# Optimization experiments

Hardware: AMD Instinct MI355X
Metric: run time of the kernel (lower is better)

Reference implementation:

```python
import jax, jax.numpy as jnp
import numpy as np

H = 16          # query heads
KV = 8          # kv heads
D = 256         # head_dim
HID = 3584      # hidden_size
ROPE_BASE = 10000.0
SCALING = 256.0 ** -0.5          # query_pre_attn_scalar ** -0.5
SOFTCAP = 50.0                   # attn_logit_softcapping
WINDOW = 1536 - 1                # sliding_window - 1 (layer_idx 0 is even)


def _rope_neox(x, positions):
    # x: [T, nh, D]; neox style: rotate the two halves of the head dim
    half = D // 2
    inv_freq = 1.0 / (ROPE_BASE ** (jnp.arange(0, D, 2, dtype=jnp.float32) / D))  # [half]
    freqs = positions.astype(jnp.float32)[:, None] * inv_freq[None, :]            # [T, half]
    cos = jnp.cos(freqs)[:, None, :]  # [T, 1, half]
    sin = jnp.sin(freqs)[:, None, :]
    x1, x2 = x[..., :half], x[..., half:]
    return jnp.concatenate([x1 * cos - x2 * sin, x2 * cos + x1 * sin], axis=-1)


def setup_inputs() -> dict:
    key = jax.random.key(0)
    k1, k2, k3 = jax.random.split(key, 3)
    T = 3072
    hidden_states = jax.random.normal(k1, (T, HID), dtype=jnp.float32)
    w_qkv = jax.random.normal(k2, (H * D + 2 * KV * D, HID), dtype=jnp.float32) * 0.02
    w_o = jax.random.normal(k3, (HID, H * D), dtype=jnp.float32) * 0.02
    positions = jnp.arange(T, dtype=jnp.int64)
    return {"positions": positions, "hidden_states": hidden_states,
            "w_qkv": w_qkv, "w_o": w_o}


def reference(positions, hidden_states, w_qkv, w_o):
    T = hidden_states.shape[0]
    qkv = hidden_states @ w_qkv.T                       # [T, (H+2KV)*D]
    q, k, v = jnp.split(qkv, [H * D, H * D + KV * D], axis=-1)
    q = q.reshape(T, H, D)
    k = k.reshape(T, KV, D)
    v = v.reshape(T, KV, D)
    q = _rope_neox(q, positions)
    k = _rope_neox(k, positions)
    # GQA: repeat kv heads (2 query heads per kv head)
    k = jnp.repeat(k, H // KV, axis=1)                  # [T, H, D]
    v = jnp.repeat(v, H // KV, axis=1)
    scores = jnp.einsum('thd,shd->hts', q, k) * SCALING  # [H, T, T]
    scores = SOFTCAP * jnp.tanh(scores / SOFTCAP)       # logit softcapping
    i = positions[:, None]
    j = positions[None, :]
    mask = (j <= i) & (i - j <= WINDOW)                 # causal + sliding window
    scores = jnp.where(mask[None, :, :], scores, -jnp.inf)
    probs = jax.nn.softmax(scores, axis=-1)
    attn = jnp.einsum('hts,shd->thd', probs, v).reshape(T, H * D)
    return attn @ w_o.T                                 # [T, HID]
```

## Files before the change

### kernel.cpp

```cpp
#include <hip/hip_runtime.h>
#include <math.h>

typedef unsigned short u16;
typedef __attribute__((ext_vector_type(8))) short short8;
typedef __attribute__((ext_vector_type(4))) float f32x4;
typedef __attribute__((ext_vector_type(4))) unsigned short u16x4;

#define HN 16
#define KVH 8
#define DH 256
#define HID 3584
#define T_LEN 3072
#define QKV_N 8192
#define O_N 4096
#define WIN 1535
#define SCALING 0.0625f
#define SOFTCAP 50.0f
#define KOFF 4096
#define VOFF 6144
#define PSTR 72
#define NJT 48
#define M_FIX 20.0f

__device__ __forceinline__ u16 f2bf(float f) {
  unsigned u = __float_as_uint(f);
  u += 0x7FFFu + ((u >> 16) & 1u);
  return (u16)(u >> 16);
}
__device__ __forceinline__ float bf2f(u16 b) {
  return __uint_as_float(((unsigned)b) << 16);
}

__device__ __forceinline__ void gload_lds16(const void* g, void* l) {
  __builtin_amdgcn_global_load_lds(
      (const __attribute__((address_space(1))) void*)g,
      (__attribute__((address_space(3))) void*)l, 16, 0, 0);
}

__device__ __forceinline__ f32x4 mfma_bf16(short8 a, short8 b, f32x4 c) {
  return __builtin_amdgcn_mfma_f32_16x16x32_bf16(a, b, c, 0, 0, 0);
}

#define BARX()                                  \
  do {                                          \
    __builtin_amdgcn_sched_barrier(0);          \
    __builtin_amdgcn_s_barrier();               \
    __builtin_amdgcn_sched_barrier(0);          \
  } while (0)

__global__ __launch_bounds__(256) void cvt2_kernel(const float* __restrict__ a,
                                                   u16* __restrict__ da, int nva,
                                                   const float* __restrict__ b,
                                                   u16* __restrict__ db, int nvb) {
  int v = blockIdx.x * 256 + threadIdx.x;
  const float* src;
  u16* dst;
  if (v < nva) {
    src = a + (size_t)v * 4;
    dst = da + (size_t)v * 4;
  } else if (v < nva + nvb) {
    int u = v - nva;
    src = b + (size_t)u * 4;
    dst = db + (size_t)u * 4;
  } else {
    return;
  }
  float4 x = *(const float4*)src;
  u16x4 o;
  o[0] = f2bf(x.x); o[1] = f2bf(x.y); o[2] = f2bf(x.z); o[3] = f2bf(x.w);
  *(u16x4*)dst = o;
}

template <int OUT_BF16>
__global__ __launch_bounds__(512, 2) void gemm8p(const u16* __restrict__ A,
                                                 const u16* __restrict__ B,
                                                 void* __restrict__ Cv,
                                                 int N, int K, int ntn, int cpx,
                                                 int gemmBlocks,
                                                 float* __restrict__ rtab) {
  __shared__ u16 sA[2][256 * 64];
  __shared__ u16 sB[2][256 * 64];

  const int bid = blockIdx.x;
  const int tid = threadIdx.x;

  if (bid >= gemmBlocks) {
    const int rb = bid - gemmBlocks;
    for (int idx = rb * 512 + tid; idx < T_LEN * 128; idx += 128 * 512) {
      int d = idx & 127;
      int t = idx >> 7;
      float inv = exp2f((float)d * (-13.287712379549449f / 128.0f));
      float ang = (float)t * inv;
      float2 cs;
      cs.x = cosf(ang);
      cs.y = sinf(ang);
      *(float2*)(rtab + (size_t)idx * 2) = cs;
    }
    return;
  }

  const int wg = (bid & 7) * cpx + (bid >> 3);
  const int bm = wg / ntn, bn = wg % ntn;
  const int row0 = bm * 256, col0 = bn * 256;
  const int lane = tid & 63, wid = tid >> 6;
  const int wr = wid >> 2, wc = wid & 3;
  const int NT = K >> 6;

  const int srow = lane >> 3;
  const int sg = (lane & 7) ^ srow;

  auto stage = [&](int tau, int kind) {
    if (tau >= NT) return;
    const int b = tau & 1;
    const int rbase = (kind & 1) * 128;
    const u16* src;
    u16* dst;
    if (kind >= 2) {
      src = A + (size_t)(row0 + rbase + wid * 8 + srow) * K + (size_t)tau * 64 + sg * 8;
      dst = &sA[b][(rbase + wid * 8) * 64];
    } else {
      src = B + (size_t)(col0 + rbase + wid * 8 + srow) * K + (size_t)tau * 64 + sg * 8;
      dst = &sB[b][(rbase + wid * 8) * 64];
    }
    gload_lds16(src, dst);
    gload_lds16(src + (size_t)64 * K, dst + 64 * 64);
  };

  f32x4 acc[8][4] = {};
  const int fr = lane & 15;
  const int fh = fr & 7;
  const int gk0 = (lane >> 4) ^ fh;
  const int gk1 = ((lane >> 4) + 4) ^ fh;

  stage(0, 0); stage(0, 1); stage(0, 2); stage(0, 3);
  stage(1, 0); stage(1, 1); stage(1, 2);
  __builtin_amdgcn_sched_barrier(0);
  asm volatile("s_waitcnt vmcnt(6)" ::: "memory");
  BARX();

  for (int u = 0; u < NT; ++u) {
    const int b = u & 1;
    const u16* pA = &sA[b][0];
    const u16* pB = &sB[b][0];
    short8 bf[4][2], afA[2][2], afB[2][2];

#define LDB_(ni, kk) (*(const short8*)&pB[(wc * 64 + (ni)*16 + fr) * 64 + (kk ? gk1 : gk0) * 8])
#define LDA_(mi, kk) (*(const short8*)&pA[(wr * 128 + (mi)*16 + fr) * 64 + (kk ? gk1 : gk0) * 8])
#define MFMA2(AF, mi0)                                                   \
  __builtin_amdgcn_s_setprio(1);                                        \
  _Pragma("unroll") for (int ni = 0; ni < 4; ++ni) {                    \
    acc[mi0][ni] = mfma_bf16(AF[0][0], bf[ni][0], acc[mi0][ni]);        \
    acc[mi0][ni] = mfma_bf16(AF[0][1], bf[ni][1], acc[mi0][ni]);        \
    acc[mi0 + 1][ni] = mfma_bf16(AF[1][0], bf[ni][0], acc[mi0 + 1][ni]);\
    acc[mi0 + 1][ni] = mfma_bf16(AF[1][1], bf[ni][1], acc[mi0 + 1][ni]);\
  }                                                                      \
  __builtin_amdgcn_s_setprio(0);                                        \
  asm volatile("s_waitcnt lgkmcnt(0)" ::: "memory");

#pragma unroll
    for (int ni = 0; ni < 4; ++ni) { bf[ni][0] = LDB_(ni, 0); bf[ni][1] = LDB_(ni, 1); }
    afA[0][0] = LDA_(0, 0); afA[0][1] = LDA_(0, 1);
    afA[1][0] = LDA_(1, 0); afA[1][1] = LDA_(1, 1);
    stage(u + 1, 3);
    BARX();
    MFMA2(afA, 0);
    BARX();
    afA[0][0] = LDA_(2, 0); afA[0][1] = LDA_(2, 1);
    afA[1][0] = LDA_(3, 0); afA[1][1] = LDA_(3, 1);
    stage(u + 2, 0);
    BARX();
    MFMA2(afA, 2);
    BARX();
    afA[0][0] = LDA_(4, 0); afA[0][1] = LDA_(4, 1);
    afA[1][0] = LDA_(5, 0); afA[1][1] = LDA_(5, 1);
    afB[0][0] = LDA_(6, 0); afB[0][1] = LDA_(6, 1);
    afB[1][0] = LDA_(7, 0); afB[1][1] = LDA_(7, 1);
    stage(u + 2, 1);
    BARX();
    MFMA2(afA, 4);
    BARX();
    stage(u + 2, 2);
    __builtin_amdgcn_sched_barrier(0);
    if (u + 2 < NT) {
      asm volatile("s_waitcnt vmcnt(6)" ::: "memory");
    } else {
      asm volatile("s_waitcnt vmcnt(0)" ::: "memory");
    }
    BARX();
    MFMA2(afB, 6);
    BARX();
#undef LDB_
#undef LDA_
#undef MFMA2
  }

#pragma unroll
  for (int mi = 0; mi < 8; ++mi) {
#pragma unroll
    for (int ni = 0; ni < 4; ++ni) {
      const int r = row0 + wr * 128 + mi * 16 + (lane >> 4) * 4;
      const int c = col0 + wc * 64 + ni * 16 + (lane & 15);
#pragma unroll
      for (int j = 0; j < 4; ++j) {
        float v = acc[mi][ni][j];
        if (OUT_BF16)
          ((u16*)Cv)[(size_t)(r + j) * N + c] = f2bf(v);
        else
          ((float*)Cv)[(size_t)(r + j) * N + c] = v;
      }
    }
  }
}

__global__ __launch_bounds__(256) void rope_kernel(u16* __restrict__ qkv,
                                                   const float* __restrict__ tab) {
  int idx = blockIdx.x * 256 + threadIdx.x;
  int d = idx & 127;
  int hh = (idx >> 7) % 24;
  int t = idx / (24 * 128);
  if (t >= T_LEN) return;
  size_t base = (size_t)t * QKV_N + (hh < HN ? hh * DH : HN * DH + (hh - HN) * DH);
  float2 cs = *(const float2*)(tab + ((size_t)(t << 7) + d) * 2);
  float x1 = bf2f(qkv[base + d]);
  float x2 = bf2f(qkv[base + d + 128]);
  qkv[base + d] = f2bf(x1 * cs.x - x2 * cs.y);
  qkv[base + d + 128] = f2bf(x2 * cs.x + x1 * cs.y);
}

__global__ __launch_bounds__(256) void vtrans_kernel(const u16* __restrict__ qkv,
                                                     u16* __restrict__ vt) {
  __shared__ u16 tile[256 * 72];
  const int jb = blockIdx.x * 64;
  const int kvh = blockIdx.y;
  const int tid = threadIdx.x;
  const int t = tid & 63, dc = tid >> 6;

  const u16* src = qkv + (size_t)(jb + t) * QKV_N + VOFF + kvh * DH + dc * 64;
#pragma unroll
  for (int i = 0; i < 8; ++i) {
    short8 v = *(const short8*)(src + i * 8);
    int d0 = dc * 64 + i * 8;
#pragma unroll
    for (int j = 0; j < 8; ++j) tile[(d0 + j) * 72 + t] = (u16)(short)v[j];
  }
  __syncthreads();

  u16* dst = vt + ((size_t)kvh * NJT + blockIdx.x) * 16384;
#pragma unroll
  for (int s = 0; s < 8; ++s) {
    int G = s * 256 + tid;
    int d = G >> 3, g = G & 7;
    short8 x = *(const short8*)&tile[d * 72 + ((g ^ (d & 7)) * 8)];
    *(short8*)(dst + G * 8) = x;
  }
}

__global__ __launch_bounds__(256) void attn_kernel(const u16* __restrict__ qkv,
                                                   const u16* __restrict__ vt,
                                                   u16* __restrict__ po,
                                                   float* __restrict__ ml) {
  const int wg = blockIdx.x;
  const int kvh = wg & 7;
  const int rest = wg >> 3;
  const int qt = rest >> 2;
  const int c = (rest >> 1) & 1;
  const int h = kvh * 2 + (rest & 1);
  const int qb = qt * 64;
  const int tid = threadIdx.x, lane = tid & 63, w = tid >> 6;

  __shared__ u16 sK[64 * 256];
  __shared__ u16 sVt[64 * 256];
  __shared__ u16 sP[4][16 * PSTR];

  int jmin = qb - WIN; if (jmin < 0) jmin = 0;
  const int jt0 = jmin >> 6, jt1 = qb >> 6;
  const int nt = jt1 - jt0 + 1;
  const int half = (nt + 1) >> 1;
  const int t_beg = (c == 0) ? jt0 : jt0 + half;
  const int t_end = (c == 0) ? jt0 + half : jt1 + 1;

  const int qrow = qb + w * 16 + (lane & 15);
  short8 qf[8];
  {
    const u16* qp = qkv + (size_t)qrow * QKV_N + h * DH + (lane >> 4) * 8;
#pragma unroll
    for (int kc = 0; kc < 8; ++kc) qf[kc] = *(const short8*)(qp + kc * 32);
  }

  f32x4 O[16];
#pragma unroll
  for (int i = 0; i < 16; ++i) O[i] = f32x4{0.f, 0.f, 0.f, 0.f};
  float lrow[4] = {0.f, 0.f, 0.f, 0.f};

  const int dl = lane & 15;
  const int vb0 = dl * 64 + (((lane >> 4)) ^ (dl & 7)) * 8;
  const int vb1 = dl * 64 + (((lane >> 4) + 4) ^ (dl & 7)) * 8;

  for (int jt = t_beg; jt < t_end; ++jt) {
    const int jb = jt * 64;
#pragma unroll
    for (int i = 0; i < 8; ++i) {
      int rl = w * 16 + i * 2 + (lane >> 5);
      int g = (lane & 31) ^ (rl & 7);
      gload_lds16(qkv + (size_t)(jb + rl) * QKV_N + KOFF + kvh * DH + g * 8,
                  &sK[(w * 16 + i * 2) * 256]);
    }
    {
      const u16* vtile = vt + ((size_t)kvh * NJT + jt) * 16384;
#pragma unroll
      for (int s = 0; s < 8; ++s) {
        int id = w * 8 + s;
        gload_lds16(vtile + id * 512 + lane * 8, &sVt[id * 512]);
      }
    }
    __syncthreads();

    f32x4 S[4];
#pragma unroll
    for (int nf = 0; nf < 4; ++nf) S[nf] = f32x4{0.f, 0.f, 0.f, 0.f};
#pragma unroll
    for (int nf = 0; nf < 4; ++nf) {
      int krow = nf * 16 + (lane & 15);
#pragma unroll
      for (int kc = 0; kc < 8; ++kc) {
        int g = (kc * 4 + (lane >> 4)) ^ (krow & 7);
        short8 kf = *(const short8*)&sK[krow * 256 + g * 8];
        S[nf] = mfma_bf16(qf[kc], kf, S[nf]);
      }
    }

#pragma unroll
    for (int r = 0; r < 4; ++r) {
      const int irow = qb + w * 16 + (lane >> 4) * 4 + r;
      const int ql = (lane >> 4) * 4 + r;
#pragma unroll
      for (int nf = 0; nf < 4; ++nf) {
        int j = jb + nf * 16 + (lane & 15);
        float x = S[nf][r] * (SCALING / SOFTCAP);
        float e2 = __expf(-2.0f * fabsf(x));
        float th = (1.0f - e2) / (1.0f + e2);
        th = x >= 0.0f ? th : -th;
        float val = SOFTCAP * th;
        bool ok = (j <= irow) && (irow - j <= WIN);
        float p = ok ? __expf(val - M_FIX) : 0.0f;
        lrow[r] += p;
        sP[w][ql * PSTR + nf * 16 + (lane & 15)] = f2bf(p);
      }
    }

    short8 pf0 = *(const short8*)&sP[w][(lane & 15) * PSTR + (lane >> 4) * 8];
    short8 pf1 = *(const short8*)&sP[w][(lane & 15) * PSTR + 32 + (lane >> 4) * 8];
#pragma unroll
    for (int nf = 0; nf < 16; ++nf) {
      short8 vf0 = *(const short8*)&sVt[nf * 1024 + vb0];
      short8 vf1 = *(const short8*)&sVt[nf * 1024 + vb1];
      O[nf] = mfma_bf16(pf0, vf0, O[nf]);
      O[nf] = mfma_bf16(pf1, vf1, O[nf]);
    }
    __syncthreads();
  }

#pragma unroll
  for (int r = 0; r < 4; ++r) {
#pragma unroll
    for (int off = 8; off >= 1; off >>= 1) lrow[r] += __shfl_xor(lrow[r], off);
  }

#pragma unroll
  for (int nf = 0; nf < 16; ++nf) {
    int d = nf * 16 + (lane & 15);
#pragma unroll
    for (int r = 0; r < 4; ++r) {
      int trow = qb + w * 16 + (lane >> 4) * 4 + r;
      po[(((size_t)c * T_LEN + trow) * HN + h) * DH + d] = f2bf(O[nf][r]);
    }
  }
  if ((lane & 15) == 0) {
#pragma unroll
    for (int r = 0; r < 4; ++r) {
      int trow = qb + w * 16 + (lane >> 4) * 4 + r;
      size_t mi = (((size_t)c * T_LEN + trow) * HN + h) * 2;
      ml[mi] = M_FIX;
      ml[mi + 1] = lrow[r];
    }
  }
}

__global__ __launch_bounds__(256) void combine_kernel(const u16* __restrict__ po,
                                                      const float* __restrict__ ml,
                                                      u16* __restrict__ attnb,
                                                      const float* __restrict__ wo,
                                                      u16* __restrict__ wob) {
  const int t = blockIdx.x;
  const int h = threadIdx.x >> 4;
  const int d0 = (threadIdx.x & 15) * 16;
  const size_t row = (size_t)t * HN + h;
  const float l0 = ml[row * 2 + 1];
  const float l1 = ml[(size_t)T_LEN * HN * 2 + row * 2 + 1];
  const float inv = 1.0f / (l0 + l1);
  const size_t i0 = row * DH + d0;
  const size_t i1 = (size_t)T_LEN * HN * DH + i0;
#pragma unroll
  for (int half = 0; half < 2; ++half) {
    short8 x0 = *(const short8*)(po + i0 + half * 8);
    short8 x1 = *(const short8*)(po + i1 + half * 8);
    short8 o;
#pragma unroll
    for (int j = 0; j < 8; ++j)
      o[j] = (short)f2bf((bf2f((u16)x0[j]) * bf2f((u16)0x3F80) + bf2f((u16)x1[j])) * inv);
    *(short8*)(attnb + i0 + half * 8) = o;
  }

  const int nv = (HID * O_N) / 4;
  for (int v = blockIdx.x * 256 + threadIdx.x; v < nv; v += T_LEN * 256) {
    float4 x = *(const float4*)(wo + (size_t)v * 4);
    u16x4 o;
    o[0] = f2bf(x.x); o[1] = f2bf(x.y); o[2] = f2bf(x.z); o[3] = f2bf(x.w);
    *(u16x4*)(wob + (size_t)v * 4) = o;
  }
}

extern "C" void kernel_launch(void* const* d_in, const int* in_sizes, int n_in,
                              void* d_out, int out_size, void* d_ws, size_t ws_size,
                              hipStream_t stream) {
  const float* hidden = (const float*)d_in[1];
  const float* w_qkv = (const float*)d_in[2];
  const float* w_o = (const float*)d_in[3];
  float* out = (float*)d_out;
  char* ws = (char*)d_ws;

  u16* wqkvb = (u16*)(ws);
  u16* po = (u16*)(ws);
  float* ml = (float*)(ws + 50331648);
  u16* attnb = (u16*)(ws);
  u16* hb = (u16*)(ws + 58720256);
  u16* vtb = (u16*)(ws + 58720256);
  u16* qkvb = (u16*)(ws + 80740352);
  u16* wob = (u16*)(ws + 80740352);
  float* ropetab = out;

  {
    int nva = T_LEN * HID / 4;
    int nvb = QKV_N * HID / 4;
    cvt2_kernel<<<dim3((nva + nvb + 255) / 256), 256, 0, stream>>>(
        hidden, hb, nva, w_qkv, wqkvb, nvb);
  }
  gemm8p<1><<<dim3(512), 512, 0, stream>>>(hb, wqkvb, qkvb, QKV_N, HID, 32, 48,
                                           384, ropetab);
  {
    int n = T_LEN * 24 * 128;
    rope_kernel<<<dim3(n / 256), 256, 0, stream>>>(qkvb, ropetab);
  }
  vtrans_kernel<<<dim3(NJT, KVH), 256, 0, stream>>>(qkvb, vtb);
  attn_kernel<<<dim3(1536), 256, 0, stream>>>(qkvb, vtb, po, ml);
  combine_kernel<<<dim3(T_LEN), 256, 0, stream>>>(po, ml, attnb, w_o, wob);
  gemm8p<0><<<dim3(168), 512, 0, stream>>>(attnb, wob, out, HID, O_N, 14, 21,
                                           168, nullptr);
}
```

Before: 534.3 us.

## Fuse RoPE into QKV GEMM epilogue and move cos/sin table to convert kernel

Removes the standalone RoPE kernel and applies the rotation in the QKV GEMM epilogue. Each warp's B-tile columns are remapped so a thread holds both the d and d+128 halves of a head at once. The cos/sin table generation moves from extra GEMM blocks into the first blocks of the convert kernel. This drops one kernel launch and a full read/write pass over the Q/K activations. In exchange the GEMM epilogue does extra table loads and scattered stores. The combine kernel also loses a redundant multiply by one.

```diff
diff --git a/kernel.cpp b/kernel.cpp
--- a/kernel.cpp
+++ b/kernel.cpp
@@ -51,8 +51,21 @@
 __global__ __launch_bounds__(256) void cvt2_kernel(const float* __restrict__ a,
                                                    u16* __restrict__ da, int nva,
                                                    const float* __restrict__ b,
-                                                   u16* __restrict__ db, int nvb) {
-  int v = blockIdx.x * 256 + threadIdx.x;
+                                                   u16* __restrict__ db, int nvb,
+                                                   float* __restrict__ rtab) {
+  const int bid = blockIdx.x;
+  if (bid < 1536) {
+    int idx = bid * 256 + threadIdx.x;
+    int d = idx & 127;
+    int t = idx >> 7;
+    float inv = exp2f((float)d * (-13.287712379549449f / 128.0f));
+    float ang = (float)t * inv;
+    float2 cs;
+    cs.x = cosf(ang);
+    cs.y = sinf(ang);
+    *(float2*)(rtab + (size_t)idx * 2) = cs;
+  }
+  int v = bid * 256 + threadIdx.x;
   const float* src;
   u16* dst;
   if (v < nva) {
@@ -71,34 +84,17 @@
   *(u16x4*)dst = o;
 }
 
-template <int OUT_BF16>
+template <int OUT_BF16, int ROPE>
 __global__ __launch_bounds__(512, 2) void gemm8p(const u16* __restrict__ A,
                                                  const u16* __restrict__ B,
                                                  void* __restrict__ Cv,
                                                  int N, int K, int ntn, int cpx,
-                                                 int gemmBlocks,
-                                                 float* __restrict__ rtab) {
+                                                 const float* __restrict__ rtab) {
   __shared__ u16 sA[2][256 * 64];
   __shared__ u16 sB[2][256 * 64];
 
   const int bid = blockIdx.x;
   const int tid = threadIdx.x;
-
-  if (bid >= gemmBlocks) {
-    const int rb = bid - gemmBlocks;
-    for (int idx = rb * 512 + tid; idx < T_LEN * 128; idx += 128 * 512) {
-      int d = idx & 127;
-      int t = idx >> 7;
-      float inv = exp2f((float)d * (-13.287712379549449f / 128.0f));
-      float ang = (float)t * inv;
-      float2 cs;
-      cs.x = cosf(ang);
-      cs.y = sinf(ang);
-      *(float2*)(rtab + (size_t)idx * 2) = cs;
-    }
-    return;
-  }
-
   const int wg = (bid & 7) * cpx + (bid >> 3);
   const int bm = wg / ntn, bn = wg % ntn;
   const int row0 = bm * 256, col0 = bn * 256;
@@ -144,7 +140,8 @@
     const u16* pB = &sB[b][0];
     short8 bf[4][2], afA[2][2], afB[2][2];
 
-#define LDB_(ni, kk) (*(const short8*)&pB[(wc * 64 + (ni)*16 + fr) * 64 + (kk ? gk1 : gk0) * 8])
+#define CMAP(ni) (wc * 32 + ((ni) & 1) * 16 + ((ni) >> 1) * 128)
+#define LDB_(ni, kk) (*(const short8*)&pB[(CMAP(ni) + fr) * 64 + (kk ? gk1 : gk0) * 8])
 #define LDA_(mi, kk) (*(const short8*)&pA[(wr * 128 + (mi)*16 + fr) * 64 + (kk ? gk1 : gk0) * 8])
 #define MFMA2(AF, mi0)                                                   \
   __builtin_amdgcn_s_setprio(1);                                        \
@@ -194,37 +191,42 @@
 #undef MFMA2
   }
 
-#pragma unroll
-  for (int mi = 0; mi < 8; ++mi) {
-#pragma unroll
-    for (int ni = 0; ni < 4; ++ni) {
-      const int r = row0 + wr * 128 + mi * 16 + (lane >> 4) * 4;
-      const int c = col0 + wc * 64 + ni * 16 + (lane & 15);
-#pragma unroll
-      for (int j = 0; j < 4; ++j) {
-        float v = acc[mi][ni][j];
-        if (OUT_BF16)
-          ((u16*)Cv)[(size_t)(r + j) * N + c] = f2bf(v);
-        else
-          ((float*)Cv)[(size_t)(r + j) * N + c] = v;
+  if (ROPE && bn < 24) {
+#pragma unroll
+    for (int mi = 0; mi < 8; ++mi) {
+#pragma unroll
+      for (int nh = 0; nh < 2; ++nh) {
+        const int dlo = wc * 32 + nh * 16 + fr;
+#pragma unroll
+        for (int j = 0; j < 4; ++j) {
+          const int r = row0 + wr * 128 + mi * 16 + (lane >> 4) * 4 + j;
+          float2 cs = *(const float2*)(rtab + ((size_t)(r << 7) + dlo) * 2);
+          float xlo = acc[mi][nh][j];
+          float xhi = acc[mi][nh + 2][j];
+          ((u16*)Cv)[(size_t)r * N + col0 + dlo] = f2bf(xlo * cs.x - xhi * cs.y);
+          ((u16*)Cv)[(size_t)r * N + col0 + dlo + 128] = f2bf(xhi * cs.x + xlo * cs.y);
+        }
       }
     }
-  }
-}
-
-__global__ __launch_bounds__(256) void rope_kernel(u16* __restrict__ qkv,
-                                                   const float* __restrict__ tab) {
-  int idx = blockIdx.x * 256 + threadIdx.x;
-  int d = idx & 127;
-  int hh = (idx >> 7) % 24;
-  int t = idx / (24 * 128);
-  if (t >= T_LEN) return;
-  size_t base = (size_t)t * QKV_N + (hh < HN ? hh * DH : HN * DH + (hh - HN) * DH);
-  float2 cs = *(const float2*)(tab + ((size_t)(t << 7) + d) * 2);
-  float x1 = bf2f(qkv[base + d]);
-  float x2 = bf2f(qkv[base + d + 128]);
-  qkv[base + d] = f2bf(x1 * cs.x - x2 * cs.y);
-  qkv[base + d + 128] = f2bf(x2 * cs.x + x1 * cs.y);
+  } else {
+#pragma unroll
+    for (int mi = 0; mi < 8; ++mi) {
+#pragma unroll
+      for (int ni = 0; ni < 4; ++ni) {
+        const int r = row0 + wr * 128 + mi * 16 + (lane >> 4) * 4;
+        const int c = col0 + CMAP(ni) + fr;
+#pragma unroll
+        for (int j = 0; j < 4; ++j) {
+          float v = acc[mi][ni][j];
+          if (OUT_BF16)
+            ((u16*)Cv)[(size_t)(r + j) * N + c] = f2bf(v);
+          else
+            ((float*)Cv)[(size_t)(r + j) * N + c] = v;
+        }
+      }
+    }
+  }
+#undef CMAP
 }
 
 __global__ __launch_bounds__(256) void vtrans_kernel(const u16* __restrict__ qkv,
@@ -407,7 +409,7 @@
     short8 o;
 #pragma unroll
     for (int j = 0; j < 8; ++j)
-      o[j] = (short)f2bf((bf2f((u16)x0[j]) * bf2f((u16)0x3F80) + bf2f((u16)x1[j])) * inv);
+      o[j] = (short)f2bf((bf2f((u16)x0[j]) + bf2f((u16)x1[j])) * inv);
     *(short8*)(attnb + i0 + half * 8) = o;
   }
 
@@ -443,17 +445,13 @@
     int nva = T_LEN * HID / 4;
     int nvb = QKV_N * HID / 4;
     cvt2_kernel<<<dim3((nva + nvb + 255) / 256), 256, 0, stream>>>(
-        hidden, hb, nva, w_qkv, wqkvb, nvb);
-  }
-  gemm8p<1><<<dim3(512), 512, 0, stream>>>(hb, wqkvb, qkvb, QKV_N, HID, 32, 48,
-                                           384, ropetab);
-  {
-    int n = T_LEN * 24 * 128;
-    rope_kernel<<<dim3(n / 256), 256, 0, stream>>>(qkvb, ropetab);
-  }
+        hidden, hb, nva, w_qkv, wqkvb, nvb, ropetab);
+  }
+  gemm8p<1, 1><<<dim3(384), 512, 0, stream>>>(hb, wqkvb, qkvb, QKV_N, HID, 32, 48,
+                                              ropetab);
   vtrans_kernel<<<dim3(NJT, KVH), 256, 0, stream>>>(qkvb, vtb);
   attn_kernel<<<dim3(1536), 256, 0, stream>>>(qkvb, vtb, po, ml);
   combine_kernel<<<dim3(T_LEN), 256, 0, stream>>>(po, ml, attnb, w_o, wob);
-  gemm8p<0><<<dim3(168), 512, 0, stream>>>(attnb, wob, out, HID, O_N, 14, 21,
-                                           168, nullptr);
-}
+  gemm8p<0, 0><<<dim3(168), 512, 0, stream>>>(attnb, wob, out, HID, O_N, 14, 21,
+                                              nullptr);
+}
```

Result: no change. 537.5 us (+0.6%).
